# Performance work log

Hardware: AMD Instinct MI355X
Metric: run time of the kernel (lower is better)

Reference implementation:

```python
import jax, jax.numpy as jnp
import numpy as np
jax.config.update("jax_enable_x64", True)

K = 10            # num_digits
NUM_CLASSES = 10  # digit classes 0..9
EQ_TOKEN = 28
PRIMES = np.array([7, 11, 13, 17, 19, 23, 29, 31, 37], dtype=np.int64)
TWO_PI = 2.0 * np.pi
M_TOTAL = int(np.prod(PRIMES.astype(object)))  # product of primes ~2.47e11 (needs int64)
_crt = []
for p in PRIMES:
    Mi = M_TOTAL // int(p)
    _crt.append((Mi * pow(Mi, -1, int(p))) % M_TOTAL)
CRT_C = jnp.array(_crt, dtype=jnp.int64)                 # [P] CRT mixing coefficients
POW10 = jnp.array([[pow(10, k, int(p)) for k in range(K)] for p in PRIMES], dtype=jnp.float32)  # [P,K]
PR_F = jnp.array(PRIMES, dtype=jnp.float32)
PR_I = jnp.array(PRIMES, dtype=jnp.int64)
POW10_DEC = jnp.array([10 ** k for k in range(K)], dtype=jnp.int64)
_op = np.full(64, -1, dtype=np.int64)
_op[20:25] = np.arange(5)  # tokens 20..24 -> ops add,sub,mul,exp,div
OP_TABLE = jnp.array(_op)


def encode(d):
    # d [B,S,K] soft base-10 digits -> RNS circle encoding [B,S,P,2]
    theta = TWO_PI * jnp.einsum('bsk,pk->bsp', d, POW10) / PR_F
    return jnp.stack([jnp.cos(theta), jnp.sin(theta)], axis=-1)


def decode_residues(circle):
    # [B,S,P,2] -> integer residues mod p, [B,S,P] int64
    theta = jnp.arctan2(circle[..., 1], circle[..., 0])
    r = jnp.round(theta / TWO_PI * PR_F).astype(jnp.int64)
    return jnp.mod(r, PR_I)


def circle_add(a, b):
    ca, sa = a[..., 0], a[..., 1]
    cb, sb = b[..., 0], b[..., 1]
    return jnp.stack([ca * cb - sa * sb, sa * cb + ca * sb], axis=-1)


def circle_sub(a, b):
    ca, sa = a[..., 0], a[..., 1]
    cb, sb = b[..., 0], b[..., 1]
    return jnp.stack([ca * cb + sa * sb, sa * cb - ca * sb], axis=-1)


def modpow(base, exp, mod):
    # elementwise modular exponentiation, exponents < 64 (6 square-and-multiply steps)
    res = jnp.ones_like(base)
    b = jnp.mod(base, mod)
    e = exp
    for _ in range(6):
        res = jnp.where((e & 1) == 1, (res * b) % mod, res)
        b = (b * b) % mod
        e = e >> 1
    return res


def crt(residues):
    # CRT reconstruction: [B,S,P] -> [B,S] int64 in [0, M_TOTAL)
    return jnp.mod(jnp.sum(residues * CRT_C, axis=-1), M_TOTAL)


def crt_signed(residues):
    n = crt(residues)
    return jnp.where(n > M_TOTAL // 2, n - M_TOTAL, n)


def int_to_digits(n):
    # [B,S] int64 -> [B,S,K] float base-10 digits, LSB-first
    return ((n[..., None] // POW10_DEC) % 10).astype(jnp.float32)


def int_to_digits_signed(n):
    sign = (n < 0).astype(jnp.float32)[..., None]
    return jnp.concatenate([int_to_digits(jnp.abs(n)), sign], axis=-1)  # [B,S,K+1]


def decode_all_ops(a_c, b_c):
    # All 5 operations decoded to digit vectors -> [B,S,5K+1]
    ra = decode_residues(a_c)
    rb = decode_residues(b_c)
    add_d = int_to_digits(crt(decode_residues(circle_add(a_c, b_c))))
    sub_d = int_to_digits_signed(crt_signed(decode_residues(circle_sub(a_c, b_c))))
    mul_d = int_to_digits(crt((ra * rb) % PR_I))
    exp_d = int_to_digits(crt(modpow(ra, rb, PR_I)))
    inv = modpow(rb, PR_I - 2, PR_I)  # Fermat inverse
    div_r = jnp.where(rb == 0, 0, (ra * inv) % PR_I)
    div_d = int_to_digits(crt(div_r))
    return jnp.concatenate([add_d, sub_d, mul_d, exp_d, div_d], axis=-1)


def select_op(results, input_ids):
    # [B,S,5K+1] -> [B,S,K+1]: pick the relevant operation per sequence
    B, S, _ = results.shape
    pad = jnp.zeros((B, S, 1), results.dtype)
    ops = jnp.stack([
        jnp.concatenate([results[..., 0:K], pad], -1),
        results[..., K:2 * K + 1],
        jnp.concatenate([results[..., 2 * K + 1:3 * K + 1], pad], -1),
        jnp.concatenate([results[..., 3 * K + 1:4 * K + 1], pad], -1),
        jnp.concatenate([results[..., 4 * K + 1:5 * K + 1], pad], -1),
    ], axis=-2)  # [B,S,5,K+1]
    is_op = OP_TABLE[jnp.clip(input_ids, 0, 63)] >= 0
    op_pos = jnp.argmax(is_op, axis=1)  # first operator position per sequence
    op_tok = jnp.take_along_axis(input_ids, op_pos[:, None], axis=1)[:, 0]
    op_idx = OP_TABLE[jnp.clip(op_tok, 0, 63)]
    gidx = jnp.broadcast_to(jnp.clip(op_idx, 0, 4)[:, None, None, None], (B, S, 1, K + 1))
    sel = jnp.take_along_axis(ops, gidx, axis=-2)[..., 0, :]
    valid = (op_idx >= 0).astype(results.dtype)[:, None, None]
    return sel * valid


def reorder_msb(res):
    # LSB-first digits -> MSB-first, -1 sentinel past the last significant digit
    digits = res[..., :K]
    sign = res[..., K:]
    idx = jnp.arange(K)
    nz = digits != 0
    highest = jnp.max(jnp.where(nz, idx, -1), axis=-1)
    num_sig = jnp.where(jnp.any(nz, axis=-1), highest + 1, 1)
    src = jnp.clip(num_sig[..., None] - 1 - idx, 0, K - 1)
    msb = jnp.take_along_axis(digits, src, axis=-1)
    msb = jnp.where(idx < num_sig[..., None], msb, -1.0)
    return jnp.concatenate([msb, sign], axis=-1)


def setup_inputs() -> dict:
    key = jax.random.key(0)
    ks = jax.random.split(key, 6)
    B, S, D, MH = 16, 2048, 768, 128
    h = jax.random.normal(ks[0], (B, S, D), dtype=jnp.float32)
    input_ids = jax.random.randint(ks[1], (B, S), 0, 50, dtype=jnp.int64)
    W1 = jax.random.normal(ks[2], (D, MH), dtype=jnp.float32) * 0.02
    b1 = jnp.zeros((MH,), jnp.float32)
    W2 = jax.random.normal(ks[3], (MH, 2 * K * NUM_CLASSES), dtype=jnp.float32) * 0.02
    b2 = jnp.zeros((2 * K * NUM_CLASSES,), jnp.float32)
    Winj = jax.random.normal(ks[4], (K + 1, D), dtype=jnp.float32) * 0.001  # injector_init_std
    binj = jnp.zeros((D,), jnp.float32)
    gate_logit = jnp.array(-2.0, jnp.float32)  # gate_init_logit
    return {"h": h, "W1": W1, "b1": b1, "W2": W2, "b2": b2,
            "Winj": Winj, "binj": binj, "gate_logit": gate_logit, "input_ids": input_ids}


def reference(h, W1, b1, W2, b2, Winj, binj, gate_logit, input_ids):
    B, S, D = h.shape
    # OperandExtractor: per-token MLP -> soft digits for operands a and b
    hid = jax.nn.relu(h @ W1 + b1)
    logits = (hid @ W2 + b2).reshape(B, S, 2, K, NUM_CLASSES)
    probs = jax.nn.softmax(logits, axis=-1)
    dig = jnp.einsum('bsokc,c->bsok', probs, jnp.arange(NUM_CLASSES, dtype=h.dtype))
    d_a, d_b = dig[..., 0, :], dig[..., 1, :]
    # RNSCircleEncoder (frozen)
    a_c = encode(d_a)
    b_c = encode(d_b)
    # ArithmeticCompute + CRT decode: detached (torch.no_grad in original)
    results = jax.lax.stop_gradient(decode_all_ops(a_c, b_c).astype(h.dtype))
    sel = select_op(results, input_ids)
    msb = reorder_msb(sel)
    # ResultInjector: gated linear injection into the residual stream
    inj = msb @ Winj + binj
    h_prime = h + jax.nn.sigmoid(gate_logit) * inj
    # only inject for sequences containing the '=' token
    has_eq = jnp.any(input_ids == EQ_TOKEN, axis=1).astype(h.dtype)[:, None, None]
    h_prime = h + (h_prime - h) * has_eq
    return h_prime, d_a, d_b
```

## Files before the change

### kernel.cpp

```cpp
#include <hip/hip_runtime.h>

typedef unsigned short u16;
typedef unsigned int   u32;
typedef unsigned long long u64;

typedef __attribute__((ext_vector_type(8))) short short8;
typedef __attribute__((ext_vector_type(4))) float f32x4;

#define DEV static __device__ __forceinline__

__constant__ float POW10F[9][10] = {
  {1,3,2,6,4,5,1,3,2,6},
  {1,10,1,10,1,10,1,10,1,10},
  {1,10,9,12,3,4,1,10,9,12},
  {1,10,15,14,4,6,9,5,16,7},
  {1,10,5,12,6,3,11,15,17,18},
  {1,10,8,11,18,19,6,14,2,20},
  {1,10,13,14,24,8,22,17,25,18},
  {1,10,7,8,18,25,2,20,14,16},
  {1,10,26,1,10,26,1,10,26,1},
};

#define M_TOTAL  247357937827ull
#define M_HALF   123678968913ull

DEV u16 f2bf_rne(float f){
  u32 u = __float_as_uint(f);
  return (u16)((u + 0x7FFFu + ((u >> 16) & 1u)) >> 16);
}
DEV float bf2f(u16 v){ return __uint_as_float(((u32)v) << 16); }

DEV short8 pack_bf16(float4 a, float4 b){
  union { short8 s; u32 u[4]; } r;
  r.u[0] = (__float_as_uint(a.x) >> 16) | (__float_as_uint(a.y) & 0xFFFF0000u);
  r.u[1] = (__float_as_uint(a.z) >> 16) | (__float_as_uint(a.w) & 0xFFFF0000u);
  r.u[2] = (__float_as_uint(b.x) >> 16) | (__float_as_uint(b.y) & 0xFFFF0000u);
  r.u[3] = (__float_as_uint(b.z) >> 16) | (__float_as_uint(b.w) & 0xFFFF0000u);
  return r.s;
}

DEV int modpow6(int b, int e, int p){
  int res = 1; b %= p;
  #pragma unroll
  for (int i = 0; i < 6; ++i){
    if (e & 1) res = (res * b) % p;
    b = (b * b) % p;
    e >>= 1;
  }
  return res;
}

#define WAVE_SYNC() do { \
  asm volatile("s_waitcnt lgkmcnt(0)" ::: "memory"); \
  __builtin_amdgcn_sched_barrier(0); \
} while (0)

__global__ void prelude_kernel(const int* __restrict__ ids, const float* __restrict__ W1,
                               const float* __restrict__ W2, int* __restrict__ op_idx,
                               float* __restrict__ has_eq, u16* __restrict__ w1f,
                               u16* __restrict__ w2f){
  __shared__ int smin[256];
  __shared__ int seq[256];
  int bid = blockIdx.x, tid = threadIdx.x;
  if (bid < 16){
    int b = bid;
    int best = 2048, eq = 0;
    for (int i = tid; i < 2048; i += 256){
      int t = ids[b * 2048 + i];
      if (t >= 20 && t < 25) best = min(best, i);
      eq |= (t == 28) ? 1 : 0;
    }
    smin[tid] = best; seq[tid] = eq;
    __syncthreads();
    for (int s = 128; s > 0; s >>= 1){
      if (tid < s){ smin[tid] = min(smin[tid], smin[tid + s]); seq[tid] |= seq[tid + s]; }
      __syncthreads();
    }
    if (tid == 0){
      int op = -1;
      if (smin[0] < 2048) op = ids[b * 2048 + smin[0]] - 20;
      op_idx[b] = op;
      has_eq[b] = seq[0] ? 1.0f : 0.0f;
    }
  } else {
    int t = (bid - 16) * 256 + tid;
    if (t < 12288){
      int blk = t >> 6, L = t & 63;
      int T = blk >> 3, b = blk & 7;
      int q = L >> 4, ln = L & 15;
      #pragma unroll
      for (int j = 0; j < 8; ++j){
        int k = 32 * T + 8 * q + j;
        int n = 16 * b + ln;
        w1f[(size_t)blk * 512 + L * 8 + j] = f2bf_rne(W1[k * 128 + n]);
      }
    } else {
      int t2 = t - 12288;
      int blk = t2 >> 6, L = t2 & 63;
      int ts = blk / 13, b2 = blk % 13;
      int q = L >> 4, ln = L & 15;
      #pragma unroll
      for (int j = 0; j < 8; ++j){
        int k = 32 * ts + 8 * q + j;
        int n = 16 * b2 + ln;
        w2f[(size_t)blk * 512 + L * 8 + j] = (n < 200) ? f2bf_rne(W2[k * 200 + n]) : (u16)0;
      }
    }
  }
}

__launch_bounds__(256, 2)
__global__ void mega_kernel(const float* __restrict__ h, const u16* __restrict__ w1f,
                            const u16* __restrict__ w2f, const float* __restrict__ b1,
                            const float* __restrict__ b2, const float* __restrict__ Winj,
                            const float* __restrict__ binj, const float* __restrict__ gate,
                            const int* __restrict__ op_idx_ws, const float* __restrict__ has_eq_ws,
                            float* __restrict__ dout){
  __shared__ __align__(16) char lds[32768];

  const int tid  = threadIdx.x;
  const int w    = tid >> 6;
  const int lane = tid & 63;
  const int ln   = lane & 15, q = lane >> 4;
  const int wg   = blockIdx.x;
  const int tok0 = wg * 64;
  const int wtok0 = tok0 + w * 16;
  const int batch = wg >> 5;

  const int   op = op_idx_ws[batch];
  const float G  = has_eq_ws[batch] * (1.0f / (1.0f + __expf(-gate[0])));

  char*  wls      = lds + (w << 13);
  u16*   hidf     = (u16*)wls;
  u16*   logit    = (u16*)wls;
  float* digits_s = (float*)(wls + 6784);
  float* tab_s    = (float*)wls;
  u64*   ops_s    = (u64*)(wls + 1536);
  float* msbv     = (float*)(wls + 2560);

  float b1v[8];
  #pragma unroll
  for (int b = 0; b < 8; ++b) b1v[b] = b1[ln + 16 * b];

  f32x4 acc[8];
  #pragma unroll
  for (int b = 0; b < 8; ++b) acc[b] = (f32x4)0.0f;

  const float4* ap = (const float4*)(h + (size_t)(wtok0 + ln) * 768);
  float4 xa[2], xb[2];
  #pragma unroll
  for (int t = 0; t < 2; ++t){ xa[t] = ap[t * 8 + q * 2]; xb[t] = ap[t * 8 + q * 2 + 1]; }

  #pragma unroll
  for (int c = 0; c < 12; ++c){
    short8 af[2];
    #pragma unroll
    for (int t = 0; t < 2; ++t) af[t] = pack_bf16(xa[t], xb[t]);
    if (c < 11){
      const float4* ap2 = ap + (c + 1) * 16;
      #pragma unroll
      for (int t = 0; t < 2; ++t){ xa[t] = ap2[t * 8 + q * 2]; xb[t] = ap2[t * 8 + q * 2 + 1]; }
    }
    #pragma unroll
    for (int t = 0; t < 2; ++t){
      #pragma unroll
      for (int b = 0; b < 8; ++b){
        short8 bf = *(const short8*)(w1f + (size_t)(((c * 2 + t) * 8 + b)) * 512 + lane * 8);
        acc[b] = __builtin_amdgcn_mfma_f32_16x16x32_bf16(af[t], bf, acc[b], 0, 0, 0);
      }
    }
  }

  #pragma unroll
  for (int b = 0; b < 8; ++b){
    int t2 = b >> 1;
    int q2 = ((b & 1) << 1) | (ln >> 3);
    int j  = ln & 7;
    #pragma unroll
    for (int r = 0; r < 4; ++r){
      float v = fmaxf(acc[b][r] + b1v[b], 0.0f);
      int L2 = (q2 << 4) | (q * 4 + r);
      hidf[t2 * 512 + L2 * 8 + j] = (u16)(__float_as_uint(v) >> 16);
    }
  }
  WAVE_SYNC();

  short8 a2[4];
  #pragma unroll
  for (int t = 0; t < 4; ++t) a2[t] = *(const short8*)(hidf + t * 512 + lane * 8);
  WAVE_SYNC();

  float b2v[13];
  #pragma unroll
  for (int b = 0; b < 13; ++b){ int n = ln + 16 * b; b2v[b] = (n < 200) ? b2[n] : 0.0f; }
  f32x4 acc2[13];
  #pragma unroll
  for (int b = 0; b < 13; ++b) acc2[b] = (f32x4)0.0f;
  #pragma unroll
  for (int b = 0; b < 13; ++b){
    #pragma unroll
    for (int t = 0; t < 4; ++t){
      short8 bf = *(const short8*)(w2f + (size_t)(t * 13 + b) * 512 + lane * 8);
      acc2[b] = __builtin_amdgcn_mfma_f32_16x16x32_bf16(a2[t], bf, acc2[b], 0, 0, 0);
    }
  }

  #pragma unroll
  for (int b = 0; b < 13; ++b){
    #pragma unroll
    for (int r = 0; r < 4; ++r){
      float v = acc2[b][r] + b2v[b];
      logit[(q * 4 + r) * 212 + 16 * b + ln] = (u16)(__float_as_uint(v) >> 16);
    }
  }
  WAVE_SYNC();

  #pragma unroll
  for (int i = 0; i < 5; ++i){
    int task = i * 64 + lane;
    int tok = task / 20, slot = task % 20;
    const u16* lp = logit + tok * 212 + slot * 10;
    float v[10];
    #pragma unroll
    for (int k = 0; k < 10; ++k) v[k] = bf2f(lp[k]);
    float mx = v[0];
    #pragma unroll
    for (int k = 1; k < 10; ++k) mx = fmaxf(mx, v[k]);
    float s = 0.0f, sd = 0.0f;
    #pragma unroll
    for (int k = 0; k < 10; ++k){
      float e = __expf(v[k] - mx);
      s += e; sd += e * (float)k;
    }
    float dig = sd / s;
    digits_s[tok * 20 + slot] = dig;
    int gt = wtok0 + tok;
    int o = slot / 10, k10 = slot % 10;
    dout[(size_t)25165824 + (size_t)o * 327680 + (size_t)gt * 10 + k10] = dig;
  }
  WAVE_SYNC();

  #pragma unroll
  for (int i = 0; i < 5; ++i){
    int task = i * 64 + lane;
    if (task < 288){
      int tok = task / 18, rm = task % 18;
      int ab = rm / 9, pi = rm % 9;
      float t = 0.0f;
      #pragma unroll
      for (int k = 0; k < 10; ++k) t += digits_s[tok * 20 + ab * 10 + k] * POW10F[pi][k];
      tab_s[tok * 18 + ab * 9 + pi] = t;
    }
  }
  WAVE_SYNC();

  {
    constexpr int PR[9] = {7, 11, 13, 17, 19, 23, 29, 31, 37};
    constexpr u64 CRTC[9] = {
      35336848261ull, 224870852570ull, 114165202074ull, 218257003965ull,
      78113032998ull, 53773464745ull, 68236672504ull, 223420072876ull, 220616539143ull
    };
    #pragma unroll
    for (int i = 0; i < 2; ++i){
      int task = i * 64 + lane;
      if (task < 80){
        int o5 = task >> 4, tok = task & 15;
        u64 acc64 = 0;
        #pragma unroll
        for (int pi = 0; pi < 9; ++pi){
          const int p = PR[pi];
          float ta = tab_s[tok * 18 + pi], tb = tab_s[tok * 18 + 9 + pi];
          int r;
          if (o5 == 0){
            r = __float2int_rn(ta + tb) % p;
          } else if (o5 == 1){
            int s = __float2int_rn(ta - tb) % p;
            r = (s < 0) ? s + p : s;
          } else {
            int ra = __float2int_rn(ta) % p;
            int rb = __float2int_rn(tb) % p;
            if (o5 == 2) r = (ra * rb) % p;
            else if (o5 == 3) r = modpow6(ra, rb, p);
            else r = (rb == 0) ? 0 : (ra * modpow6(rb, p - 2, p)) % p;
          }
          acc64 += (u64)r * CRTC[pi];
        }
        u64 n = acc64 % M_TOTAL;
        int sign = 0;
        u64 un = n;
        if (o5 == 1 && n > M_HALF){ sign = 1; un = M_TOTAL - n; }
        u64 pk = 0;
        #pragma unroll
        for (int k = 0; k < 10; ++k){ pk |= (un % 10ull) << (4 * k); un /= 10ull; }
        pk |= ((u64)sign) << 40;
        ops_s[tok * 5 + o5] = pk;
      }
    }
  }
  WAVE_SYNC();

  if (lane < 16){
    int tok = lane;
    u64 pk = (op >= 0) ? ops_s[tok * 5 + op] : 0ull;
    int g[10]; int hi = -1;
    #pragma unroll
    for (int k = 0; k < 10; ++k){
      g[k] = (int)((pk >> (4 * k)) & 15ull);
      if (g[k] != 0) hi = k;
    }
    int ns = (hi >= 0) ? hi + 1 : 1;
    #pragma unroll
    for (int i = 0; i < 10; ++i)
      msbv[tok * 12 + i] = (i < ns) ? (float)g[ns - 1 - i] : -1.0f;
    msbv[tok * 12 + 10] = (float)((pk >> 40) & 1ull);
    msbv[tok * 12 + 11] = 0.0f;
  }
  WAVE_SYNC();

  {
    const float4* Wj4 = (const float4*)Winj;
    const float4* bj4 = (const float4*)binj;
    #pragma unroll
    for (int cc = 0; cc < 3; ++cc){
      const int f = cc * 64 + lane;
      float4 wv[11];
      #pragma unroll
      for (int j = 0; j < 11; ++j) wv[j] = Wj4[j * 192 + f];
      float4 bj = bj4[f];
      const size_t base = (size_t)wtok0 * 768 + (size_t)f * 4;
      #pragma unroll 4
      for (int row = 0; row < 16; ++row){
        float4 m0 = *(const float4*)(msbv + row * 12);
        float4 m1 = *(const float4*)(msbv + row * 12 + 4);
        float4 m2 = *(const float4*)(msbv + row * 12 + 8);
        float4 hv = *(const float4*)(h + base + (size_t)row * 768);
        float ix = bj.x, iy = bj.y, iz = bj.z, iw = bj.w;
        ix += m0.x*wv[0].x + m0.y*wv[1].x + m0.z*wv[2].x + m0.w*wv[3].x
            + m1.x*wv[4].x + m1.y*wv[5].x + m1.z*wv[6].x + m1.w*wv[7].x
            + m2.x*wv[8].x + m2.y*wv[9].x + m2.z*wv[10].x;
        iy += m0.x*wv[0].y + m0.y*wv[1].y + m0.z*wv[2].y + m0.w*wv[3].y
            + m1.x*wv[4].y + m1.y*wv[5].y + m1.z*wv[6].y + m1.w*wv[7].y
            + m2.x*wv[8].y + m2.y*wv[9].y + m2.z*wv[10].y;
        iz += m0.x*wv[0].z + m0.y*wv[1].z + m0.z*wv[2].z + m0.w*wv[3].z
            + m1.x*wv[4].z + m1.y*wv[5].z + m1.z*wv[6].z + m1.w*wv[7].z
            + m2.x*wv[8].z + m2.y*wv[9].z + m2.z*wv[10].z;
        iw += m0.x*wv[0].w + m0.y*wv[1].w + m0.z*wv[2].w + m0.w*wv[3].w
            + m1.x*wv[4].w + m1.y*wv[5].w + m1.z*wv[6].w + m1.w*wv[7].w
            + m2.x*wv[8].w + m2.y*wv[9].w + m2.z*wv[10].w;
        float4 o;
        o.x = hv.x + G * ix; o.y = hv.y + G * iy;
        o.z = hv.z + G * iz; o.w = hv.w + G * iw;
        *(float4*)(dout + base + (size_t)row * 768) = o;
      }
    }
  }
}

extern "C" void kernel_launch(void* const* d_in, const int* in_sizes, int n_in,
                              void* d_out, int out_size, void* d_ws, size_t ws_size,
                              hipStream_t stream){
  const float* h    = (const float*)d_in[0];
  const float* W1   = (const float*)d_in[1];
  const float* b1   = (const float*)d_in[2];
  const float* W2   = (const float*)d_in[3];
  const float* b2   = (const float*)d_in[4];
  const float* Winj = (const float*)d_in[5];
  const float* binj = (const float*)d_in[6];
  const float* gate = (const float*)d_in[7];
  const int*   ids  = (const int*)d_in[8];
  float* dout = (float*)d_out;

  char* ws = (char*)d_ws;
  int*   op_idx = (int*)(ws + 0);
  float* has_eq = (float*)(ws + 64);
  u16*   w1f    = (u16*)(ws + 256);
  u16*   w2f    = (u16*)(ws + 256 + 196608);

  prelude_kernel<<<77, 256, 0, stream>>>(ids, W1, W2, op_idx, has_eq, w1f, w2f);
  mega_kernel<<<512, 256, 0, stream>>>(h, w1f, w2f, b1, b2, Winj, binj, gate,
                                       op_idx, has_eq, dout);
}
```

Measured before the change: 240.1 us.

## Split each 16-token tile across two waves sharing GEMM columns via LDS

Changes the work split from 4 waves with 16 tokens each (512 blocks of 256 threads) to 2 waves per 16-token tile (2048 blocks of 128 threads). The two waves split the hidden and logit GEMM columns and share results through LDS with block barriers, then each wave handles 8 tokens for the softmax, CRT and injection stages. LDS use drops from 32 KB to about 11 KB and per-wave accumulator registers are halved, which allows more resident blocks and finer-grained parallelism. The cost is that the h activation tile is loaded by both waves, two __syncthreads are added, and the 13 logit column blocks split unevenly (7 and 6).

```diff
diff --git a/kernel.cpp b/kernel.cpp
--- a/kernel.cpp
+++ b/kernel.cpp
@@ -109,44 +109,43 @@
   }
 }
 
-__launch_bounds__(256, 2)
+__launch_bounds__(128, 4)
 __global__ void mega_kernel(const float* __restrict__ h, const u16* __restrict__ w1f,
                             const u16* __restrict__ w2f, const float* __restrict__ b1,
                             const float* __restrict__ b2, const float* __restrict__ Winj,
                             const float* __restrict__ binj, const float* __restrict__ gate,
                             const int* __restrict__ op_idx_ws, const float* __restrict__ has_eq_ws,
                             float* __restrict__ dout){
-  __shared__ __align__(16) char lds[32768];
+  __shared__ __align__(16) char lds[10880];
+  u16* hidf  = (u16*)lds;
+  u16* logit = (u16*)(lds + 4096);
 
   const int tid  = threadIdx.x;
   const int w    = tid >> 6;
   const int lane = tid & 63;
   const int ln   = lane & 15, q = lane >> 4;
   const int wg   = blockIdx.x;
-  const int tok0 = wg * 64;
-  const int wtok0 = tok0 + w * 16;
-  const int batch = wg >> 5;
+  const int tok0 = wg * 16;
+  const int batch = wg >> 7;
 
   const int   op = op_idx_ws[batch];
   const float G  = has_eq_ws[batch] * (1.0f / (1.0f + __expf(-gate[0])));
 
-  char*  wls      = lds + (w << 13);
-  u16*   hidf     = (u16*)wls;
-  u16*   logit    = (u16*)wls;
-  float* digits_s = (float*)(wls + 6784);
-  float* tab_s    = (float*)wls;
-  u64*   ops_s    = (u64*)(wls + 1536);
-  float* msbv     = (float*)(wls + 2560);
-
-  float b1v[8];
-  #pragma unroll
-  for (int b = 0; b < 8; ++b) b1v[b] = b1[ln + 16 * b];
-
-  f32x4 acc[8];
-  #pragma unroll
-  for (int b = 0; b < 8; ++b) acc[b] = (f32x4)0.0f;
-
-  const float4* ap = (const float4*)(h + (size_t)(wtok0 + ln) * 768);
+  char*  wls      = lds + (w << 11);
+  float* digits_s = (float*)wls;
+  float* tab_s    = (float*)(wls + 640);
+  u64*   ops_s    = (u64*)(wls + 1216);
+  float* msbv     = (float*)(wls + 1536);
+
+  float b1v[4];
+  #pragma unroll
+  for (int b = 0; b < 4; ++b) b1v[b] = b1[w * 64 + 16 * b + ln];
+
+  f32x4 acc[4];
+  #pragma unroll
+  for (int b = 0; b < 4; ++b) acc[b] = (f32x4)0.0f;
+
+  const float4* ap = (const float4*)(h + (size_t)(tok0 + ln) * 768);
   float4 xa[2], xb[2];
   #pragma unroll
   for (int t = 0; t < 2; ++t){ xa[t] = ap[t * 8 + q * 2]; xb[t] = ap[t * 8 + q * 2 + 1]; }
@@ -164,17 +163,18 @@
     #pragma unroll
     for (int t = 0; t < 2; ++t){
       #pragma unroll
-      for (int b = 0; b < 8; ++b){
-        short8 bf = *(const short8*)(w1f + (size_t)(((c * 2 + t) * 8 + b)) * 512 + lane * 8);
+      for (int b = 0; b < 4; ++b){
+        short8 bf = *(const short8*)(w1f + (size_t)((c * 2 + t) * 8 + w * 4 + b) * 512 + lane * 8);
         acc[b] = __builtin_amdgcn_mfma_f32_16x16x32_bf16(af[t], bf, acc[b], 0, 0, 0);
       }
     }
   }
 
   #pragma unroll
-  for (int b = 0; b < 8; ++b){
-    int t2 = b >> 1;
-    int q2 = ((b & 1) << 1) | (ln >> 3);
+  for (int b = 0; b < 4; ++b){
+    int nb = w * 4 + b;
+    int t2 = nb >> 1;
+    int q2 = ((nb & 1) << 1) | (ln >> 3);
     int j  = ln & 7;
     #pragma unroll
     for (int r = 0; r < 4; ++r){
@@ -183,73 +183,85 @@
       hidf[t2 * 512 + L2 * 8 + j] = (u16)(__float_as_uint(v) >> 16);
     }
   }
+  __syncthreads();
+
+  short8 a2[4];
+  #pragma unroll
+  for (int t = 0; t < 4; ++t) a2[t] = *(const short8*)(hidf + t * 512 + lane * 8);
+
+  const int nstart = w * 7;
+  const int ncnt   = 7 - w;
+  float b2v[7];
+  #pragma unroll
+  for (int bb = 0; bb < 7; ++bb){
+    int n = (nstart + bb) * 16 + ln;
+    b2v[bb] = (bb < ncnt && n < 200) ? b2[n] : 0.0f;
+  }
+  f32x4 acc2[7];
+  #pragma unroll
+  for (int bb = 0; bb < 7; ++bb) acc2[bb] = (f32x4)0.0f;
+  #pragma unroll
+  for (int bb = 0; bb < 7; ++bb){
+    if (bb < ncnt){
+      #pragma unroll
+      for (int t = 0; t < 4; ++t){
+        short8 bf = *(const short8*)(w2f + (size_t)(t * 13 + nstart + bb) * 512 + lane * 8);
+        acc2[bb] = __builtin_amdgcn_mfma_f32_16x16x32_bf16(a2[t], bf, acc2[bb], 0, 0, 0);
+      }
+    }
+  }
+
+  #pragma unroll
+  for (int bb = 0; bb < 7; ++bb){
+    if (bb < ncnt){
+      #pragma unroll
+      for (int r = 0; r < 4; ++r){
+        float v = acc2[bb][r] + b2v[bb];
+        logit[(q * 4 + r) * 212 + (nstart + bb) * 16 + ln] = (u16)(__float_as_uint(v) >> 16);
+      }
+    }
+  }
+  __syncthreads();
+
+
+  #pragma unroll
+  for (int i = 0; i < 3; ++i){
+    int task = i * 64 + lane;
+    if (task < 160){
+      int tl = task / 20, slot = task % 20;
+      int tok = w * 8 + tl;
+      const u16* lp = logit + tok * 212 + slot * 10;
+      float v[10];
+      #pragma unroll
+      for (int k = 0; k < 10; ++k) v[k] = bf2f(lp[k]);
+      float mx = v[0];
+      #pragma unroll
+      for (int k = 1; k < 10; ++k) mx = fmaxf(mx, v[k]);
+      float s = 0.0f, sd = 0.0f;
+      #pragma unroll
+      for (int k = 0; k < 10; ++k){
+        float e = __expf(v[k] - mx);
+        s += e; sd += e * (float)k;
+      }
+      float dig = sd / s;
+      digits_s[tl * 20 + slot] = dig;
+      int gt = tok0 + tok;
+      int o = slot / 10, k10 = slot % 10;
+      dout[(size_t)25165824 + (size_t)o * 327680 + (size_t)gt * 10 + k10] = dig;
+    }
+  }
   WAVE_SYNC();
 
-  short8 a2[4];
-  #pragma unroll
-  for (int t = 0; t < 4; ++t) a2[t] = *(const short8*)(hidf + t * 512 + lane * 8);
-  WAVE_SYNC();
-
-  float b2v[13];
-  #pragma unroll
-  for (int b = 0; b < 13; ++b){ int n = ln + 16 * b; b2v[b] = (n < 200) ? b2[n] : 0.0f; }
-  f32x4 acc2[13];
-  #pragma unroll
-  for (int b = 0; b < 13; ++b) acc2[b] = (f32x4)0.0f;
-  #pragma unroll
-  for (int b = 0; b < 13; ++b){
-    #pragma unroll
-    for (int t = 0; t < 4; ++t){
-      short8 bf = *(const short8*)(w2f + (size_t)(t * 13 + b) * 512 + lane * 8);
-      acc2[b] = __builtin_amdgcn_mfma_f32_16x16x32_bf16(a2[t], bf, acc2[b], 0, 0, 0);
-    }
-  }
-
-  #pragma unroll
-  for (int b = 0; b < 13; ++b){
-    #pragma unroll
-    for (int r = 0; r < 4; ++r){
-      float v = acc2[b][r] + b2v[b];
-      logit[(q * 4 + r) * 212 + 16 * b + ln] = (u16)(__float_as_uint(v) >> 16);
-    }
-  }
-  WAVE_SYNC();
-
-  #pragma unroll
-  for (int i = 0; i < 5; ++i){
+  #pragma unroll
+  for (int i = 0; i < 3; ++i){
     int task = i * 64 + lane;
-    int tok = task / 20, slot = task % 20;
-    const u16* lp = logit + tok * 212 + slot * 10;
-    float v[10];
-    #pragma unroll
-    for (int k = 0; k < 10; ++k) v[k] = bf2f(lp[k]);
-    float mx = v[0];
-    #pragma unroll
-    for (int k = 1; k < 10; ++k) mx = fmaxf(mx, v[k]);
-    float s = 0.0f, sd = 0.0f;
-    #pragma unroll
-    for (int k = 0; k < 10; ++k){
-      float e = __expf(v[k] - mx);
-      s += e; sd += e * (float)k;
-    }
-    float dig = sd / s;
-    digits_s[tok * 20 + slot] = dig;
-    int gt = wtok0 + tok;
-    int o = slot / 10, k10 = slot % 10;
-    dout[(size_t)25165824 + (size_t)o * 327680 + (size_t)gt * 10 + k10] = dig;
-  }
-  WAVE_SYNC();
-
-  #pragma unroll
-  for (int i = 0; i < 5; ++i){
-    int task = i * 64 + lane;
-    if (task < 288){
-      int tok = task / 18, rm = task % 18;
+    if (task < 144){
+      int tl = task / 18, rm = task % 18;
       int ab = rm / 9, pi = rm % 9;
       float t = 0.0f;
       #pragma unroll
-      for (int k = 0; k < 10; ++k) t += digits_s[tok * 20 + ab * 10 + k] * POW10F[pi][k];
-      tab_s[tok * 18 + ab * 9 + pi] = t;
+      for (int k = 0; k < 10; ++k) t += digits_s[tl * 20 + ab * 10 + k] * POW10F[pi][k];
+      tab_s[tl * 18 + ab * 9 + pi] = t;
     }
   }
   WAVE_SYNC();
@@ -260,48 +272,44 @@
       35336848261ull, 224870852570ull, 114165202074ull, 218257003965ull,
       78113032998ull, 53773464745ull, 68236672504ull, 223420072876ull, 220616539143ull
     };
-    #pragma unroll
-    for (int i = 0; i < 2; ++i){
-      int task = i * 64 + lane;
-      if (task < 80){
-        int o5 = task >> 4, tok = task & 15;
-        u64 acc64 = 0;
-        #pragma unroll
-        for (int pi = 0; pi < 9; ++pi){
-          const int p = PR[pi];
-          float ta = tab_s[tok * 18 + pi], tb = tab_s[tok * 18 + 9 + pi];
-          int r;
-          if (o5 == 0){
-            r = __float2int_rn(ta + tb) % p;
-          } else if (o5 == 1){
-            int s = __float2int_rn(ta - tb) % p;
-            r = (s < 0) ? s + p : s;
-          } else {
-            int ra = __float2int_rn(ta) % p;
-            int rb = __float2int_rn(tb) % p;
-            if (o5 == 2) r = (ra * rb) % p;
-            else if (o5 == 3) r = modpow6(ra, rb, p);
-            else r = (rb == 0) ? 0 : (ra * modpow6(rb, p - 2, p)) % p;
-          }
-          acc64 += (u64)r * CRTC[pi];
+    if (lane < 40){
+      int o5 = lane >> 3, tl = lane & 7;
+      u64 acc64 = 0;
+      #pragma unroll
+      for (int pi = 0; pi < 9; ++pi){
+        const int p = PR[pi];
+        float ta = tab_s[tl * 18 + pi], tb = tab_s[tl * 18 + 9 + pi];
+        int r;
+        if (o5 == 0){
+          r = __float2int_rn(ta + tb) % p;
+        } else if (o5 == 1){
+          int s = __float2int_rn(ta - tb) % p;
+          r = (s < 0) ? s + p : s;
+        } else {
+          int ra = __float2int_rn(ta) % p;
+          int rb = __float2int_rn(tb) % p;
+          if (o5 == 2) r = (ra * rb) % p;
+          else if (o5 == 3) r = modpow6(ra, rb, p);
+          else r = (rb == 0) ? 0 : (ra * modpow6(rb, p - 2, p)) % p;
         }
-        u64 n = acc64 % M_TOTAL;
-        int sign = 0;
-        u64 un = n;
-        if (o5 == 1 && n > M_HALF){ sign = 1; un = M_TOTAL - n; }
-        u64 pk = 0;
-        #pragma unroll
-        for (int k = 0; k < 10; ++k){ pk |= (un % 10ull) << (4 * k); un /= 10ull; }
-        pk |= ((u64)sign) << 40;
-        ops_s[tok * 5 + o5] = pk;
-      }
+        acc64 += (u64)r * CRTC[pi];
+      }
+      u64 n = acc64 % M_TOTAL;
+      int sign = 0;
+      u64 un = n;
+      if (o5 == 1 && n > M_HALF){ sign = 1; un = M_TOTAL - n; }
+      u64 pk = 0;
+      #pragma unroll
+      for (int k = 0; k < 10; ++k){ pk |= (un % 10ull) << (4 * k); un /= 10ull; }
+      pk |= ((u64)sign) << 40;
+      ops_s[tl * 5 + o5] = pk;
     }
   }
   WAVE_SYNC();
 
-  if (lane < 16){
-    int tok = lane;
-    u64 pk = (op >= 0) ? ops_s[tok * 5 + op] : 0ull;
+  if (lane < 8){
+    int tl = lane;
+    u64 pk = (op >= 0) ? ops_s[tl * 5 + op] : 0ull;
     int g[10]; int hi = -1;
     #pragma unroll
     for (int k = 0; k < 10; ++k){
@@ -311,9 +319,9 @@
     int ns = (hi >= 0) ? hi + 1 : 1;
     #pragma unroll
     for (int i = 0; i < 10; ++i)
-      msbv[tok * 12 + i] = (i < ns) ? (float)g[ns - 1 - i] : -1.0f;
-    msbv[tok * 12 + 10] = (float)((pk >> 40) & 1ull);
-    msbv[tok * 12 + 11] = 0.0f;
+      msbv[tl * 12 + i] = (i < ns) ? (float)g[ns - 1 - i] : -1.0f;
+    msbv[tl * 12 + 10] = (float)((pk >> 40) & 1ull);
+    msbv[tl * 12 + 11] = 0.0f;
   }
   WAVE_SYNC();
 
@@ -327,9 +335,9 @@
       #pragma unroll
       for (int j = 0; j < 11; ++j) wv[j] = Wj4[j * 192 + f];
       float4 bj = bj4[f];
-      const size_t base = (size_t)wtok0 * 768 + (size_t)f * 4;
+      const size_t base = (size_t)(tok0 + w * 8) * 768 + (size_t)f * 4;
       #pragma unroll 4
-      for (int row = 0; row < 16; ++row){
+      for (int row = 0; row < 8; ++row){
         float4 m0 = *(const float4*)(msbv + row * 12);
         float4 m1 = *(const float4*)(msbv + row * 12 + 4);
         float4 m2 = *(const float4*)(msbv + row * 12 + 8);
@@ -377,6 +385,6 @@
   u16*   w2f    = (u16*)(ws + 256 + 196608);
 
   prelude_kernel<<<77, 256, 0, stream>>>(ids, W1, W2, op_idx, has_eq, w1f, w2f);
-  mega_kernel<<<512, 256, 0, stream>>>(h, w1f, w2f, b1, b2, Winj, binj, gate,
-                                       op_idx, has_eq, dout);
-}
+  mega_kernel<<<2048, 128, 0, stream>>>(h, w1f, w2f, b1, b2, Winj, binj, gate,
+                                        op_idx, has_eq, dout);
+}
```

New measurement: 338.4 us. +41.0%, slower.
